# Performance work log

Hardware: AMD Instinct MI355X
Metric: run time of the kernel (lower is better)

Reference implementation:

```python
import jax, jax.numpy as jnp
import numpy as np

N_ATOMS = 100_000
N_EDGES = 1_600_000
N_RADIAL = 16
N_ELEM = 119          # periodic table size used by per-element scale/shift
HIDDEN = 512
N_FEAT = N_RADIAL + N_RADIAL * N_RADIAL  # M0 + M1-contraction features = 272
R_CUT = 5.0
EPS = 1e-8


def setup_inputs() -> dict:
    key = jax.random.key(0)
    ks = jax.random.split(key, 10)
    R = jax.random.normal(ks[0], (N_ATOMS, 3), jnp.float32)
    Z = jax.random.randint(ks[1], (N_ATOMS,), 0, N_ELEM).astype(jnp.int32)
    idx = jax.random.randint(ks[2], (2, N_EDGES), 0, N_ATOMS)
    box = jnp.zeros((3, 3), jnp.float32)
    offsets = jnp.zeros((N_EDGES, 3), jnp.float32)
    # descriptor params: Gaussian radial basis centers / width
    centers = jnp.linspace(0.0, R_CUT, N_RADIAL, dtype=jnp.float32)
    width = jnp.asarray(0.5, jnp.float32)
    # readout MLP params
    W1 = jax.random.normal(ks[3], (N_FEAT, HIDDEN), jnp.float32) / np.sqrt(N_FEAT)
    b1 = jnp.zeros((HIDDEN,), jnp.float32)
    W2 = jax.random.normal(ks[4], (HIDDEN, HIDDEN), jnp.float32) / np.sqrt(HIDDEN)
    b2 = jnp.zeros((HIDDEN,), jnp.float32)
    W3 = jax.random.normal(ks[5], (HIDDEN, 1), jnp.float32) / np.sqrt(HIDDEN)
    b3 = jnp.zeros((1,), jnp.float32)
    # per-element scale/shift
    scale = jnp.ones((N_ELEM,), jnp.float32)
    shift = jax.random.normal(ks[6], (N_ELEM,), jnp.float32)
    return {"R": R, "Z": Z, "idx": idx, "box": box, "offsets": offsets,
            "centers": centers, "width": width,
            "W1": W1, "b1": b1, "W2": W2, "b2": b2, "W3": W3, "b3": b3,
            "scale": scale, "shift": shift}


def reference(R, Z, idx, box, offsets, centers, width,
              W1, b1, W2, b2, W3, b3, scale, shift):
    n = R.shape[0]
    idx_i, idx_j = idx[0], idx[1]
    # edge gather + free displacement (init_box == 0): dr = displacement(Rj, Ri) = Rj - Ri
    dr = R[idx_j] - R[idx_i]                      # (E, 3)
    r = jnp.linalg.norm(dr, axis=-1, keepdims=True)  # (E, 1)
    d = dr / (r + EPS)                            # unit directions (E, 3)
    # Gaussian radial basis (E, K)
    b = jnp.exp(-((r - centers[None, :]) ** 2) / (2.0 * width * width))
    # scatter-sum moments per atom
    M0 = jax.ops.segment_sum(b, idx_i, num_segments=n)                       # (N, K)
    M1 = jax.ops.segment_sum(b[:, :, None] * d[:, None, :], idx_i,
                             num_segments=n)                                 # (N, K, 3)
    # rotation-invariant gaussian-moment contraction
    G1 = jnp.einsum('nad,nbd->nab', M1, M1).reshape(n, -1)                   # (N, K*K)
    feat = jnp.concatenate([M0, G1], axis=-1)                                # (N, 272)
    # per-atom readout MLP (swish)
    h = jax.nn.silu(feat @ W1 + b1)
    h = jax.nn.silu(h @ W2 + b2)
    h = h @ W3 + b3                                                          # (N, 1)
    # per-element scale/shift, then total energy
    atomic_energies = scale[Z][:, None] * h + shift[Z][:, None]
    return jnp.sum(atomic_energies)
```

## Files before the change

kernel.cpp:

```cpp
#include <hip/hip_runtime.h>
#include <hip/hip_bf16.h>
#include <cstdint>

#define HID 512
#define K1P 288

typedef __attribute__((ext_vector_type(8))) short bf16x8;
typedef __attribute__((ext_vector_type(4))) float f32x4;

__device__ __forceinline__ short f2bf(float x) {
    __hip_bfloat16 h = __float2bfloat16(x);
    return *(short*)&h;
}
__device__ __forceinline__ float silu(float x) {
    return x * (1.0f / (1.0f + __expf(-x)));
}
__device__ __forceinline__ void gl_lds16(const void* src, void* dst) {
    __builtin_amdgcn_global_load_lds(
        (const __attribute__((address_space(1))) void*)src,
        (__attribute__((address_space(3))) void*)dst, 16, 0, 0);
}
__device__ __forceinline__ int xcd_swz(int bid, int nwg) {
    int q = nwg >> 3, r = nwg & 7;
    int xcd = bid & 7, i = bid >> 3;
    int base = (xcd < r) ? xcd * (q + 1) : r * (q + 1) + (xcd - r) * q;
    return base + i;
}

__global__ __launch_bounds__(256) void hist_kernel(
    const int* __restrict__ idx, int* __restrict__ counts, int nEdges)
{
    int e = blockIdx.x * 256 + threadIdx.x;
    if (e < nEdges) atomicAdd(&counts[idx[e]], 1);
}

__global__ __launch_bounds__(1024) void scan1_kernel(
    const int* __restrict__ counts, int* __restrict__ starts,
    int* __restrict__ blockSum, int n)
{
    __shared__ int wsum[16];
    int t = threadIdx.x, lane = t & 63, wid = t >> 6;
    int i = blockIdx.x * 1024 + t;
    int v = (i < n) ? counts[i] : 0;
    int incl = v;
    #pragma unroll
    for (int off = 1; off < 64; off <<= 1) {
        int u = __shfl_up(incl, off);
        if (lane >= off) incl += u;
    }
    if (lane == 63) wsum[wid] = incl;
    __syncthreads();
    if (t < 16) {
        int s = wsum[t];
        #pragma unroll
        for (int off = 1; off < 16; off <<= 1) {
            int u = __shfl_up(s, off);
            if (t >= off) s += u;
        }
        wsum[t] = s;
    }
    __syncthreads();
    int woff = (wid == 0) ? 0 : wsum[wid - 1];
    if (i < n) starts[i] = woff + incl - v;
    if (t == 0) blockSum[blockIdx.x] = wsum[15];
}

__global__ __launch_bounds__(1024) void scan2_kernel(
    const int* __restrict__ blockSum, int* __restrict__ blockOff,
    int* __restrict__ starts, int nb, int n)
{
    __shared__ int arr[1024];
    int t = threadIdx.x;
    int v = (t < nb) ? blockSum[t] : 0;
    arr[t] = v;
    __syncthreads();
    #pragma unroll
    for (int off = 1; off < 1024; off <<= 1) {
        int x = (t >= off) ? arr[t - off] : 0;
        __syncthreads();
        arr[t] += x;
        __syncthreads();
    }
    if (t < nb) blockOff[t] = arr[t] - v;
    if (t == 0) starts[n] = arr[nb - 1];
}

__global__ __launch_bounds__(1024) void scan3_kernel(
    int* __restrict__ starts, int* __restrict__ cursor,
    const int* __restrict__ blockOff, int n)
{
    int i = blockIdx.x * 1024 + threadIdx.x;
    if (i < n) {
        int s = starts[i] + blockOff[blockIdx.x];
        starts[i] = s;
        cursor[i] = s;
    }
}

__global__ __launch_bounds__(256) void scatter_kernel(
    const float* __restrict__ R, const int* __restrict__ idx,
    int* __restrict__ cursor, float4* __restrict__ sorted, int nEdges)
{
    int e = blockIdx.x * 256 + threadIdx.x;
    if (e >= nEdges) return;
    int i = idx[e];
    int j = idx[nEdges + e];
    float rix = R[3*(size_t)i], riy = R[3*(size_t)i+1], riz = R[3*(size_t)i+2];
    float rjx = R[3*(size_t)j], rjy = R[3*(size_t)j+1], rjz = R[3*(size_t)j+2];
    float dx = rjx - rix, dy = rjy - riy, dz = rjz - riz;
    float r = sqrtf(dx*dx + dy*dy + dz*dz);
    float inv = 1.0f / (r + 1e-8f);
    int pos = atomicAdd(&cursor[i], 1);
    sorted[pos] = make_float4(r, dx*inv, dy*inv, dz*inv);
}

__global__ __launch_bounds__(256) void accum_kernel(
    const float4* __restrict__ sorted, const int* __restrict__ starts,
    const float* __restrict__ centers, const float* __restrict__ width,
    float* __restrict__ M0M1, int nAtoms)
{
    int wv = threadIdx.x >> 6, lane = threadIdx.x & 63;
    int atom = blockIdx.x * 4 + wv;
    if (atom >= nAtoms) return;
    int s = starts[atom], e = starts[atom + 1];
    int k = lane >> 2, c = lane & 3;
    float ck = centers[k];
    float w = width[0];
    float inv2w2 = 1.0f / (2.0f * w * w);
    float acc = 0.0f;
    auto term = [&](float4 v) {
        float diff = v.x - ck;
        float b = __expf(-diff * diff * inv2w2);
        float comp = (c == 0) ? 1.0f : ((c == 1) ? v.y : ((c == 2) ? v.z : v.w));
        return b * comp;
    };
    int p = s;
    for (; p + 3 < e; p += 4) {
        float4 v0 = sorted[p];
        float4 v1 = sorted[p + 1];
        float4 v2 = sorted[p + 2];
        float4 v3 = sorted[p + 3];
        acc += term(v0); acc += term(v1); acc += term(v2); acc += term(v3);
    }
    for (; p < e; ++p) acc += term(sorted[p]);
    M0M1[(size_t)atom * 64 + lane] = acc;
}

__global__ __launch_bounds__(256) void convW_kernel(
    const float* __restrict__ W, short* __restrict__ Wt, int K, int Kpad, int N)
{
    int n = blockIdx.x * 256 + threadIdx.x;
    int k = blockIdx.y;
    if (n >= N) return;
    float v = (k < K) ? W[(size_t)k * N + n] : 0.0f;
    Wt[(size_t)n * Kpad + k] = f2bf(v);
}

__global__ __launch_bounds__(256, 2) void gemm1_mfma(
    const float* __restrict__ M0M1, const short* __restrict__ W1t,
    const float* __restrict__ bias, short* __restrict__ C, int M, int nwg)
{
    __shared__ float MsT[64][128];
    __shared__ short Asl[2][4096];
    __shared__ short Bsl[4][4096];
    int t = threadIdx.x;
    int w = t >> 6, lane = t & 63;
    int wr = w >> 1, wc = w & 1;
    int li = lane & 15, lg = lane >> 4;
    int lin = xcd_swz(blockIdx.x, nwg);
    int row0 = (lin >> 2) * 128;
    int col0 = (lin & 3) * 128;

    {
        int mrow = t >> 1, mo = (t & 1) * 32;
        int gm = row0 + mrow; if (gm > M - 1) gm = M - 1;
        const float4* src = (const float4*)(M0M1 + (size_t)gm * 64 + mo);
        #pragma unroll
        for (int q = 0; q < 8; ++q) {
            float4 v = src[q];
            int c0 = mo + q * 4;
            MsT[c0+0][mrow] = v.x; MsT[c0+1][mrow] = v.y;
            MsT[c0+2][mrow] = v.z; MsT[c0+3][mrow] = v.w;
        }
    }
    __syncthreads();

    auto stageA = [&](int kt, int buf) {
        #pragma unroll
        for (int p = 0; p < 2; ++p) {
            int cell = p * 256 + t;
            int k8 = cell >> 7, row = cell & 127;
            int kbase = kt * 32 + k8 * 8;
            bf16x8 v;
            if (kbase < 16) {
                #pragma unroll
                for (int j = 0; j < 8; ++j) v[j] = f2bf(MsT[4*(kbase+j)][row]);
            } else if (kbase < 272) {
                int g = kbase - 16, a = g >> 4, b0 = g & 15;
                float ax = MsT[4*a+1][row], ay = MsT[4*a+2][row], az = MsT[4*a+3][row];
                #pragma unroll
                for (int j = 0; j < 8; ++j) {
                    int b = b0 + j;
                    v[j] = f2bf(ax*MsT[4*b+1][row] + ay*MsT[4*b+2][row] + az*MsT[4*b+3][row]);
                }
            } else {
                #pragma unroll
                for (int j = 0; j < 8; ++j) v[j] = 0;
            }
            *(bf16x8*)&Asl[buf][cell * 8] = v;
        }
    };
    auto stageB = [&](int kt, int buf) {
        #pragma unroll
        for (int p = 0; p < 2; ++p) {
            int cell = p * 256 + t;
            int k8 = cell >> 7, col = cell & 127;
            const short* src = W1t + (size_t)(col0 + col) * K1P + kt*32 + k8*8;
            gl_lds16(src, &Bsl[buf][(p * 256 + w * 64) * 8]);
        }
    };

    f32x4 acc[4][4] = {};
    const int NS = K1P / 32;
    stageA(0, 0);
    stageB(0, 0); stageB(1, 1); stageB(2, 2);

    #pragma unroll
    for (int s = 0; s < NS; ++s) {
        if (s <= NS - 3)      asm volatile("s_waitcnt vmcnt(4) lgkmcnt(0)\n\ts_barrier" ::: "memory");
        else if (s == NS - 2) asm volatile("s_waitcnt vmcnt(2) lgkmcnt(0)\n\ts_barrier" ::: "memory");
        else                  asm volatile("s_waitcnt vmcnt(0) lgkmcnt(0)\n\ts_barrier" ::: "memory");
        if (s + 3 < NS) stageB(s + 3, (s + 3) & 3);
        bf16x8 af[4], bfr[4];
        #pragma unroll
        for (int m = 0; m < 4; ++m)
            af[m] = *(const bf16x8*)&Asl[s & 1][(lg*128 + wr*64 + m*16 + li) * 8];
        #pragma unroll
        for (int n = 0; n < 4; ++n)
            bfr[n] = *(const bf16x8*)&Bsl[s & 3][(lg*128 + wc*64 + n*16 + li) * 8];
        if (s + 1 < NS) stageA(s + 1, (s + 1) & 1);
        __builtin_amdgcn_s_setprio(1);
        #pragma unroll
        for (int m = 0; m < 4; ++m)
            #pragma unroll
            for (int n = 0; n < 4; ++n)
                acc[m][n] = __builtin_amdgcn_mfma_f32_16x16x32_bf16(af[m], bfr[n], acc[m][n], 0, 0, 0);
        __builtin_amdgcn_s_setprio(0);
    }

    float bv[4];
    #pragma unroll
    for (int n = 0; n < 4; ++n) bv[n] = bias[col0 + wc*64 + n*16 + li];
    #pragma unroll
    for (int m = 0; m < 4; ++m)
        #pragma unroll
        for (int r = 0; r < 4; ++r) {
            int row = row0 + wr*64 + m*16 + lg*4 + r;
            if (row >= M) continue;
            size_t base = (size_t)row * HID + col0 + wc*64 + li;
            #pragma unroll
            for (int n = 0; n < 4; ++n) {
                float cx = acc[m][n][r] + bv[n];
                C[base + n*16] = f2bf(silu(cx));
            }
        }
}

__global__ __launch_bounds__(256, 2) void gemm2_mfma(
    const short* __restrict__ A, const short* __restrict__ W2t,
    const float* __restrict__ bias, const float* __restrict__ W3,
    const float* __restrict__ b3, const float* __restrict__ scale,
    const float* __restrict__ shift, const int* __restrict__ Z,
    float* __restrict__ out, int M, int nwg)
{
    __shared__ short Asl[4][4096];
    __shared__ short Bsl[4][4096];
    __shared__ float rsum[2][128];
    __shared__ float red[4];
    int t = threadIdx.x;
    int w = t >> 6, lane = t & 63;
    int wr = w >> 1, wc = w & 1;
    int li = lane & 15, lg = lane >> 4;
    int lin = xcd_swz(blockIdx.x, nwg);
    int row0 = (lin >> 2) * 128;
    int col0 = (lin & 3) * 128;

    auto stage = [&](int kt, int buf) {
        #pragma unroll
        for (int p = 0; p < 2; ++p) {
            int cell = p * 256 + t;
            int k8 = cell >> 7, row = cell & 127;
            int gr = row0 + row; if (gr > M - 1) gr = M - 1;
            const short* src = A + (size_t)gr * HID + kt*32 + k8*8;
            gl_lds16(src, &Asl[buf][(p * 256 + w * 64) * 8]);
        }
        #pragma unroll
        for (int p = 0; p < 2; ++p) {
            int cell = p * 256 + t;
            int k8 = cell >> 7, col = cell & 127;
            const short* src = W2t + (size_t)(col0 + col) * HID + kt*32 + k8*8;
            gl_lds16(src, &Bsl[buf][(p * 256 + w * 64) * 8]);
        }
    };

    f32x4 acc[4][4] = {};
    const int NS = HID / 32;
    stage(0, 0); stage(1, 1); stage(2, 2);

    for (int s = 0; s < NS; ++s) {
        if (s <= NS - 3)      asm volatile("s_waitcnt vmcnt(8)\n\ts_barrier" ::: "memory");
        else if (s == NS - 2) asm volatile("s_waitcnt vmcnt(4)\n\ts_barrier" ::: "memory");
        else                  asm volatile("s_waitcnt vmcnt(0)\n\ts_barrier" ::: "memory");
        if (s + 3 < NS) stage(s + 3, (s + 3) & 3);
        bf16x8 af[4], bfr[4];
        #pragma unroll
        for (int m = 0; m < 4; ++m)
            af[m] = *(const bf16x8*)&Asl[s & 3][(lg*128 + wr*64 + m*16 + li) * 8];
        #pragma unroll
        for (int n = 0; n < 4; ++n)
            bfr[n] = *(const bf16x8*)&Bsl[s & 3][(lg*128 + wc*64 + n*16 + li) * 8];
        __builtin_amdgcn_s_setprio(1);
        #pragma unroll
        for (int m = 0; m < 4; ++m)
            #pragma unroll
            for (int n = 0; n < 4; ++n)
                acc[m][n] = __builtin_amdgcn_mfma_f32_16x16x32_bf16(af[m], bfr[n], acc[m][n], 0, 0, 0);
        __builtin_amdgcn_s_setprio(0);
    }

    float bv[4], w3v[4];
    #pragma unroll
    for (int n = 0; n < 4; ++n) {
        int col = col0 + wc*64 + n*16 + li;
        bv[n]  = bias[col];
        w3v[n] = W3[col];
    }
    #pragma unroll
    for (int m = 0; m < 4; ++m)
        #pragma unroll
        for (int r = 0; r < 4; ++r) {
            float s = 0.f;
            #pragma unroll
            for (int n = 0; n < 4; ++n) {
                float cx = acc[m][n][r] + bv[n];
                s += silu(cx) * w3v[n];
            }
            #pragma unroll
            for (int off = 1; off < 16; off <<= 1) s += __shfl_xor(s, off);
            if (li == 0) rsum[wc][wr*64 + m*16 + lg*4 + r] = s;
        }
    __syncthreads();
    float e = 0.f;
    if (t < 128) {
        int row = row0 + t;
        if (row < M) {
            float v = rsum[0][t] + rsum[1][t];
            int z = Z[row];
            e = scale[z] * v;
            if ((lin & 3) == 0) e += scale[z] * b3[0] + shift[z];
        }
    }
    #pragma unroll
    for (int off = 32; off > 0; off >>= 1) e += __shfl_down(e, off);
    if (lane == 0) red[w] = e;
    __syncthreads();
    if (t == 0) atomicAdd(out, red[0] + red[1] + red[2] + red[3]);
}

extern "C" void kernel_launch(void* const* d_in, const int* in_sizes, int n_in,
                              void* d_out, int out_size, void* d_ws, size_t ws_size,
                              hipStream_t stream)
{
    const float* R       = (const float*)d_in[0];
    const int*   Z       = (const int*)  d_in[1];
    const int*   idx     = (const int*)  d_in[2];
    const float* centers = (const float*)d_in[5];
    const float* width   = (const float*)d_in[6];
    const float* W1      = (const float*)d_in[7];
    const float* b1      = (const float*)d_in[8];
    const float* W2      = (const float*)d_in[9];
    const float* b2      = (const float*)d_in[10];
    const float* W3      = (const float*)d_in[11];
    const float* b3      = (const float*)d_in[12];
    const float* scale   = (const float*)d_in[13];
    const float* shift   = (const float*)d_in[14];

    int nAtoms = in_sizes[0] / 3;
    int nEdges = in_sizes[2] / 2;

    size_t m0m1_b = (size_t)nAtoms * 64 * sizeof(float);
    size_t h1_b   = (size_t)nAtoms * HID * 2;
    size_t w1t_b  = (size_t)HID * K1P * 2;
    size_t w2t_b  = (size_t)HID * HID * 2;
    if (ws_size < m0m1_b + h1_b + w1t_b + w2t_b) return;

    char* ws = (char*)d_ws;
    float* M0M1 = (float*)ws;
    char*  regB = ws + m0m1_b;
    short* h1   = (short*)regB;
    short* W1t  = (short*)(ws + m0m1_b + h1_b);
    short* W2t  = W1t + (size_t)HID * K1P;

    int nb = (nAtoms + 1023) / 1024;
    size_t sorted_b = (size_t)nEdges * sizeof(float4);
    float4* sorted = (float4*)regB;
    int* counts   = (int*)(regB + sorted_b);
    int* starts   = counts + nAtoms;
    int* cursor   = starts + nAtoms + 1;
    int* blockSum = cursor + nAtoms;
    int* blockOff = blockSum + nb;
    if (sorted_b + (size_t)(3 * nAtoms + 1 + 2 * nb) * sizeof(int) > h1_b) return;

    float* out = (float*)d_out;

    hipMemsetAsync(counts, 0, (size_t)nAtoms * sizeof(int), stream);
    hipMemsetAsync(out, 0, sizeof(float), stream);

    convW_kernel<<<dim3(2, K1P), 256, 0, stream>>>(W1, W1t, 272, K1P, HID);
    convW_kernel<<<dim3(2, HID), 256, 0, stream>>>(W2, W2t, HID, HID, HID);

    int eb = (nEdges + 255) / 256;
    hist_kernel <<<eb, 256, 0, stream>>>(idx, counts, nEdges);
    scan1_kernel<<<nb, 1024, 0, stream>>>(counts, starts, blockSum, nAtoms);
    scan2_kernel<<<1, 1024, 0, stream>>>(blockSum, blockOff, starts, nb, nAtoms);
    scan3_kernel<<<nb, 1024, 0, stream>>>(starts, cursor, blockOff, nAtoms);
    scatter_kernel<<<eb, 256, 0, stream>>>(R, idx, cursor, sorted, nEdges);
    accum_kernel<<<(nAtoms + 3) / 4, 256, 0, stream>>>(sorted, starts, centers, width, M0M1, nAtoms);

    int gb = (nAtoms + 127) / 128;
    int nwg = gb * 4;
    gemm1_mfma<<<nwg, 256, 0, stream>>>(M0M1, W1t, b1, h1, nAtoms, nwg);
    gemm2_mfma<<<nwg, 256, 0, stream>>>(h1, W2t, b2, W3, b3, scale, shift, Z, out, nAtoms, nwg);
}
```

Baseline: 476.0 us.

## Make gemm2 persistent with LDS-resident W2 slice and register-streamed A rows

Replaces the tiled, multi-buffered gemm2 with a persistent kernel of 256 blocks of 512 threads. Each block loads its full 128-column slice of W2 (128 KB) into LDS once and then loops over row tiles. Each wave streams its own 16 A rows directly from global memory into registers, prefetching the next tile's first K chunks. This removes the per-tile LDS staging of both operands and the block barriers. Per-row energies are accumulated in registers and committed with one atomic per wave. The cost is a large LDS footprint (one block per CU) and uncoalesced per-lane A loads that bypass LDS.

```diff
diff --git a/kernel.cpp b/kernel.cpp
--- a/kernel.cpp
+++ b/kernel.cpp
@@ -266,105 +266,101 @@
         }
 }
 
-__global__ __launch_bounds__(256, 2) void gemm2_mfma(
+__global__ __launch_bounds__(512, 1) void gemm2_bres(
     const short* __restrict__ A, const short* __restrict__ W2t,
     const float* __restrict__ bias, const float* __restrict__ W3,
     const float* __restrict__ b3, const float* __restrict__ scale,
     const float* __restrict__ shift, const int* __restrict__ Z,
-    float* __restrict__ out, int M, int nwg)
-{
-    __shared__ short Asl[4][4096];
-    __shared__ short Bsl[4][4096];
-    __shared__ float rsum[2][128];
-    __shared__ float red[4];
+    float* __restrict__ out, int M, int T)
+{
+    __shared__ short Bp[8192 * 8];
     int t = threadIdx.x;
     int w = t >> 6, lane = t & 63;
-    int wr = w >> 1, wc = w & 1;
     int li = lane & 15, lg = lane >> 4;
-    int lin = xcd_swz(blockIdx.x, nwg);
-    int row0 = (lin >> 2) * 128;
+    int lin = xcd_swz(blockIdx.x, 256);
     int col0 = (lin & 3) * 128;
-
-    auto stage = [&](int kt, int buf) {
-        #pragma unroll
-        for (int p = 0; p < 2; ++p) {
-            int cell = p * 256 + t;
-            int k8 = cell >> 7, row = cell & 127;
-            int gr = row0 + row; if (gr > M - 1) gr = M - 1;
-            const short* src = A + (size_t)gr * HID + kt*32 + k8*8;
-            gl_lds16(src, &Asl[buf][(p * 256 + w * 64) * 8]);
-        }
-        #pragma unroll
-        for (int p = 0; p < 2; ++p) {
-            int cell = p * 256 + t;
-            int k8 = cell >> 7, col = cell & 127;
-            const short* src = W2t + (size_t)(col0 + col) * HID + kt*32 + k8*8;
-            gl_lds16(src, &Bsl[buf][(p * 256 + w * 64) * 8]);
-        }
-    };
-
-    f32x4 acc[4][4] = {};
-    const int NS = HID / 32;
-    stage(0, 0); stage(1, 1); stage(2, 2);
-
-    for (int s = 0; s < NS; ++s) {
-        if (s <= NS - 3)      asm volatile("s_waitcnt vmcnt(8)\n\ts_barrier" ::: "memory");
-        else if (s == NS - 2) asm volatile("s_waitcnt vmcnt(4)\n\ts_barrier" ::: "memory");
-        else                  asm volatile("s_waitcnt vmcnt(0)\n\ts_barrier" ::: "memory");
-        if (s + 3 < NS) stage(s + 3, (s + 3) & 3);
-        bf16x8 af[4], bfr[4];
-        #pragma unroll
-        for (int m = 0; m < 4; ++m)
-            af[m] = *(const bf16x8*)&Asl[s & 3][(lg*128 + wr*64 + m*16 + li) * 8];
-        #pragma unroll
-        for (int n = 0; n < 4; ++n)
-            bfr[n] = *(const bf16x8*)&Bsl[s & 3][(lg*128 + wc*64 + n*16 + li) * 8];
-        __builtin_amdgcn_s_setprio(1);
-        #pragma unroll
-        for (int m = 0; m < 4; ++m)
-            #pragma unroll
-            for (int n = 0; n < 4; ++n)
-                acc[m][n] = __builtin_amdgcn_mfma_f32_16x16x32_bf16(af[m], bfr[n], acc[m][n], 0, 0, 0);
-        __builtin_amdgcn_s_setprio(0);
-    }
-
-    float bv[4], w3v[4];
-    #pragma unroll
-    for (int n = 0; n < 4; ++n) {
-        int col = col0 + wc*64 + n*16 + li;
+    int rg = lin >> 2;
+
+    #pragma unroll
+    for (int i = 0; i < 16; ++i) {
+        int cell = i * 512 + t;
+        int c = cell >> 9, k8 = (cell >> 7) & 3, col = cell & 127;
+        const short* src = W2t + (size_t)(col0 + col) * HID + c * 32 + k8 * 8;
+        gl_lds16(src, &Bp[(i * 512 + w * 64) * 8]);
+    }
+    asm volatile("s_waitcnt vmcnt(0)" ::: "memory");
+    __syncthreads();
+
+    float bv[8], w3v[8];
+    #pragma unroll
+    for (int n = 0; n < 8; ++n) {
+        int col = col0 + n * 16 + li;
         bv[n]  = bias[col];
         w3v[n] = W3[col];
     }
-    #pragma unroll
-    for (int m = 0; m < 4; ++m)
+    float b30 = b3[0];
+    float ew = 0.f;
+
+    const short* arowCur;
+    {
+        int gr = rg * 128 + w * 16 + li; if (gr > M - 1) gr = M - 1;
+        arowCur = A + (size_t)gr * HID + lg * 8;
+    }
+    bf16x8 aw0 = *(const bf16x8*)(arowCur +  0);
+    bf16x8 aw1 = *(const bf16x8*)(arowCur + 32);
+    bf16x8 aw2 = *(const bf16x8*)(arowCur + 64);
+    bf16x8 aw3 = *(const bf16x8*)(arowCur + 96);
+
+    for (int rt = rg; rt < T; rt += 64) {
+        int row0w = rt * 128 + w * 16;
+        const short* arowNext;
+        {
+            int rtn = (rt + 64 < T) ? rt + 64 : rt;
+            int gr = rtn * 128 + w * 16 + li; if (gr > M - 1) gr = M - 1;
+            arowNext = A + (size_t)gr * HID + lg * 8;
+        }
+        f32x4 acc[8] = {};
+        #pragma unroll
+        for (int kt = 0; kt < 16; ++kt) {
+            bf16x8 a = (kt & 3) == 0 ? aw0 : (kt & 3) == 1 ? aw1 : (kt & 3) == 2 ? aw2 : aw3;
+            bf16x8 bfr[8];
+            #pragma unroll
+            for (int n = 0; n < 8; ++n)
+                bfr[n] = *(const bf16x8*)&Bp[((kt*4 + lg)*128 + n*16 + li) * 8];
+            bf16x8 nxt;
+            if (kt < 12) nxt = *(const bf16x8*)(arowCur + (kt + 4) * 32);
+            else         nxt = *(const bf16x8*)(arowNext + (kt - 12) * 32);
+            #pragma unroll
+            for (int n = 0; n < 8; ++n)
+                acc[n] = __builtin_amdgcn_mfma_f32_16x16x32_bf16(a, bfr[n], acc[n], 0, 0, 0);
+            if ((kt & 3) == 0) aw0 = nxt; else if ((kt & 3) == 1) aw1 = nxt;
+            else if ((kt & 3) == 2) aw2 = nxt; else aw3 = nxt;
+        }
+        arowCur = arowNext;
         #pragma unroll
         for (int r = 0; r < 4; ++r) {
             float s = 0.f;
             #pragma unroll
-            for (int n = 0; n < 4; ++n) {
-                float cx = acc[m][n][r] + bv[n];
+            for (int n = 0; n < 8; ++n) {
+                float cx = acc[n][r] + bv[n];
                 s += silu(cx) * w3v[n];
             }
-            #pragma unroll
-            for (int off = 1; off < 16; off <<= 1) s += __shfl_xor(s, off);
-            if (li == 0) rsum[wc][wr*64 + m*16 + lg*4 + r] = s;
-        }
-    __syncthreads();
-    float e = 0.f;
-    if (t < 128) {
-        int row = row0 + t;
-        if (row < M) {
-            float v = rsum[0][t] + rsum[1][t];
-            int z = Z[row];
-            e = scale[z] * v;
-            if ((lin & 3) == 0) e += scale[z] * b3[0] + shift[z];
-        }
-    }
-    #pragma unroll
-    for (int off = 32; off > 0; off >>= 1) e += __shfl_down(e, off);
-    if (lane == 0) red[w] = e;
-    __syncthreads();
-    if (t == 0) atomicAdd(out, red[0] + red[1] + red[2] + red[3]);
+            s += __shfl_xor(s, 1);
+            s += __shfl_xor(s, 2);
+            s += __shfl_xor(s, 4);
+            s += __shfl_xor(s, 8);
+            int row = row0w + lg*4 + r;
+            if (li == 0 && row < M) {
+                int z = Z[row];
+                float e = scale[z] * s;
+                if (col0 == 0) e += scale[z] * b30 + shift[z];
+                ew += e;
+            }
+        }
+    }
+    #pragma unroll
+    for (int off = 32; off > 0; off >>= 1) ew += __shfl_down(ew, off);
+    if (lane == 0) atomicAdd(out, ew);
 }
 
 extern "C" void kernel_launch(void* const* d_in, const int* in_sizes, int n_in,
@@ -430,5 +426,6 @@
     int gb = (nAtoms + 127) / 128;
     int nwg = gb * 4;
     gemm1_mfma<<<nwg, 256, 0, stream>>>(M0M1, W1t, b1, h1, nAtoms, nwg);
-    gemm2_mfma<<<nwg, 256, 0, stream>>>(h1, W2t, b2, W3, b3, scale, shift, Z, out, nAtoms, nwg);
-}
+    int T = gb;
+    gemm2_bres<<<256, 512, 0, stream>>>(h1, W2t, b2, W3, b3, scale, shift, Z, out, nAtoms, T);
+}
```

Result: slower. 873.3 us (+83.5%).

## Double-buffer MFMA operand registers and deepen LDS prefetch in both GEMMs

Applied to the files above, without the earlier changes.

Both GEMM kernels now load the next k-step's A/B fragments from LDS into a second register buffer while the current step's MFMAs run. The aim is to hide LDS read latency behind matrix math. gemm1 gets a third A LDS buffer so A can be staged two steps ahead, and the vmcnt waits are tightened to match. This raises register and LDS use, which may lower occupancy, and the waits must cover the earlier reads.

```diff
diff --git a/kernel.cpp b/kernel.cpp
--- a/kernel.cpp
+++ b/kernel.cpp
@@ -161,7 +161,7 @@
     const float* __restrict__ bias, short* __restrict__ C, int M, int nwg)
 {
     __shared__ float MsT[64][128];
-    __shared__ short Asl[2][4096];
+    __shared__ short Asl[3][4096];
     __shared__ short Bsl[4][4096];
     int t = threadIdx.x;
     int w = t >> 6, lane = t & 63;
@@ -221,30 +221,38 @@
     };
 
     f32x4 acc[4][4] = {};
+    bf16x8 afs[2][4], bfs[2][4];
     const int NS = K1P / 32;
-    stageA(0, 0);
+    stageA(0, 0); stageA(1, 1);
     stageB(0, 0); stageB(1, 1); stageB(2, 2);
+    asm volatile("s_waitcnt vmcnt(4) lgkmcnt(0)\n\ts_barrier" ::: "memory");
+    #pragma unroll
+    for (int m = 0; m < 4; ++m)
+        afs[0][m] = *(const bf16x8*)&Asl[0][(lg*128 + wr*64 + m*16 + li) * 8];
+    #pragma unroll
+    for (int n = 0; n < 4; ++n)
+        bfs[0][n] = *(const bf16x8*)&Bsl[0][(lg*128 + wc*64 + n*16 + li) * 8];
 
     #pragma unroll
     for (int s = 0; s < NS; ++s) {
-        if (s <= NS - 3)      asm volatile("s_waitcnt vmcnt(4) lgkmcnt(0)\n\ts_barrier" ::: "memory");
-        else if (s == NS - 2) asm volatile("s_waitcnt vmcnt(2) lgkmcnt(0)\n\ts_barrier" ::: "memory");
-        else                  asm volatile("s_waitcnt vmcnt(0) lgkmcnt(0)\n\ts_barrier" ::: "memory");
+        if (s <= NS - 3) asm volatile("s_waitcnt vmcnt(2) lgkmcnt(0)\n\ts_barrier" ::: "memory");
+        else             asm volatile("s_waitcnt vmcnt(0) lgkmcnt(0)\n\ts_barrier" ::: "memory");
         if (s + 3 < NS) stageB(s + 3, (s + 3) & 3);
-        bf16x8 af[4], bfr[4];
+        if (s + 2 < NS) stageA(s + 2, (s + 2) % 3);
+        if (s + 1 < NS) {
+            #pragma unroll
+            for (int m = 0; m < 4; ++m)
+                afs[(s+1)&1][m] = *(const bf16x8*)&Asl[(s+1) % 3][(lg*128 + wr*64 + m*16 + li) * 8];
+            #pragma unroll
+            for (int n = 0; n < 4; ++n)
+                bfs[(s+1)&1][n] = *(const bf16x8*)&Bsl[(s+1) & 3][(lg*128 + wc*64 + n*16 + li) * 8];
+        }
+        __builtin_amdgcn_s_setprio(1);
         #pragma unroll
         for (int m = 0; m < 4; ++m)
-            af[m] = *(const bf16x8*)&Asl[s & 1][(lg*128 + wr*64 + m*16 + li) * 8];
-        #pragma unroll
-        for (int n = 0; n < 4; ++n)
-            bfr[n] = *(const bf16x8*)&Bsl[s & 3][(lg*128 + wc*64 + n*16 + li) * 8];
-        if (s + 1 < NS) stageA(s + 1, (s + 1) & 1);
-        __builtin_amdgcn_s_setprio(1);
-        #pragma unroll
-        for (int m = 0; m < 4; ++m)
             #pragma unroll
             for (int n = 0; n < 4; ++n)
-                acc[m][n] = __builtin_amdgcn_mfma_f32_16x16x32_bf16(af[m], bfr[n], acc[m][n], 0, 0, 0);
+                acc[m][n] = __builtin_amdgcn_mfma_f32_16x16x32_bf16(afs[s&1][m], bfs[s&1][n], acc[m][n], 0, 0, 0);
         __builtin_amdgcn_s_setprio(0);
     }
 
@@ -304,27 +312,36 @@
     };
 
     f32x4 acc[4][4] = {};
+    bf16x8 afs[2][4], bfs[2][4];
     const int NS = HID / 32;
     stage(0, 0); stage(1, 1); stage(2, 2);
-
+    asm volatile("s_waitcnt vmcnt(8)\n\ts_barrier" ::: "memory");
+    #pragma unroll
+    for (int m = 0; m < 4; ++m)
+        afs[0][m] = *(const bf16x8*)&Asl[0][(lg*128 + wr*64 + m*16 + li) * 8];
+    #pragma unroll
+    for (int n = 0; n < 4; ++n)
+        bfs[0][n] = *(const bf16x8*)&Bsl[0][(lg*128 + wc*64 + n*16 + li) * 8];
+
+    #pragma unroll
     for (int s = 0; s < NS; ++s) {
-        if (s <= NS - 3)      asm volatile("s_waitcnt vmcnt(8)\n\ts_barrier" ::: "memory");
-        else if (s == NS - 2) asm volatile("s_waitcnt vmcnt(4)\n\ts_barrier" ::: "memory");
-        else                  asm volatile("s_waitcnt vmcnt(0)\n\ts_barrier" ::: "memory");
+        if (s <= NS - 3) asm volatile("s_waitcnt vmcnt(4)\n\ts_barrier" ::: "memory");
+        else             asm volatile("s_waitcnt vmcnt(0)\n\ts_barrier" ::: "memory");
         if (s + 3 < NS) stage(s + 3, (s + 3) & 3);
-        bf16x8 af[4], bfr[4];
+        if (s + 1 < NS) {
+            #pragma unroll
+            for (int m = 0; m < 4; ++m)
+                afs[(s+1)&1][m] = *(const bf16x8*)&Asl[(s+1) & 3][(lg*128 + wr*64 + m*16 + li) * 8];
+            #pragma unroll
+            for (int n = 0; n < 4; ++n)
+                bfs[(s+1)&1][n] = *(const bf16x8*)&Bsl[(s+1) & 3][(lg*128 + wc*64 + n*16 + li) * 8];
+        }
+        __builtin_amdgcn_s_setprio(1);
         #pragma unroll
         for (int m = 0; m < 4; ++m)
-            af[m] = *(const bf16x8*)&Asl[s & 3][(lg*128 + wr*64 + m*16 + li) * 8];
-        #pragma unroll
-        for (int n = 0; n < 4; ++n)
-            bfr[n] = *(const bf16x8*)&Bsl[s & 3][(lg*128 + wc*64 + n*16 + li) * 8];
-        __builtin_amdgcn_s_setprio(1);
-        #pragma unroll
-        for (int m = 0; m < 4; ++m)
             #pragma unroll
             for (int n = 0; n < 4; ++n)
-                acc[m][n] = __builtin_amdgcn_mfma_f32_16x16x32_bf16(af[m], bfr[n], acc[m][n], 0, 0, 0);
+                acc[m][n] = __builtin_amdgcn_mfma_f32_16x16x32_bf16(afs[s&1][m], bfs[s&1][n], acc[m][n], 0, 0, 0);
         __builtin_amdgcn_s_setprio(0);
     }
 
```

Result: slower. 523.1 us (+9.9%).

## Fuse moment contraction into accum kernel and feed bf16 features to GEMM1

Applied to the files above, without the earlier changes.

The accum kernel now builds the full 288-wide bf16 feature row (M0 plus the M1·M1 contraction) per atom through shared memory and writes it to a new workspace buffer. A new gemm_feat kernel streams that buffer with a 4-stage global_load_lds pipeline, replacing gemm1's on-the-fly feature construction from fp32 M0M1. This removes the contraction work that was redundant across the four column tiles of GEMM1, at the cost of writing and reading an extra ~57MB of features. The path only runs if the workspace is large enough, otherwise it falls back to the old code.

```diff
diff --git a/kernel.cpp b/kernel.cpp
--- a/kernel.cpp
+++ b/kernel.cpp
@@ -117,8 +117,10 @@
 __global__ __launch_bounds__(256) void accum_kernel(
     const float4* __restrict__ sorted, const int* __restrict__ starts,
     const float* __restrict__ centers, const float* __restrict__ width,
-    float* __restrict__ M0M1, int nAtoms)
-{
+    float* __restrict__ M0M1, short* __restrict__ feat16,
+    int nAtoms, int useFeat)
+{
+    __shared__ float sm[4][64];
     int wv = threadIdx.x >> 6, lane = threadIdx.x & 63;
     int atom = blockIdx.x * 4 + wv;
     if (atom >= nAtoms) return;
@@ -143,7 +145,31 @@
         acc += term(v0); acc += term(v1); acc += term(v2); acc += term(v3);
     }
     for (; p < e; ++p) acc += term(sorted[p]);
-    M0M1[(size_t)atom * 64 + lane] = acc;
+
+    if (!useFeat) {
+        M0M1[(size_t)atom * 64 + lane] = acc;
+        return;
+    }
+    sm[wv][lane] = acc;
+    asm volatile("s_waitcnt lgkmcnt(0)" ::: "memory");
+    short* frow = feat16 + (size_t)atom * K1P;
+    #pragma unroll
+    for (int q = 0; q < 5; ++q) {
+        int idx5 = q * 64 + lane;
+        if (idx5 >= K1P) break;
+        float val;
+        if (idx5 < 16) {
+            val = sm[wv][4 * idx5];
+        } else if (idx5 < 272) {
+            int g = idx5 - 16, a = g >> 4, b = g & 15;
+            val = sm[wv][4*a+1] * sm[wv][4*b+1]
+                + sm[wv][4*a+2] * sm[wv][4*b+2]
+                + sm[wv][4*a+3] * sm[wv][4*b+3];
+        } else {
+            val = 0.0f;
+        }
+        frow[idx5] = f2bf(val);
+    }
 }
 
 __global__ __launch_bounds__(256) void convW_kernel(
@@ -266,6 +292,82 @@
         }
 }
 
+__global__ __launch_bounds__(256, 2) void gemm_feat(
+    const short* __restrict__ F, const short* __restrict__ W1t,
+    const float* __restrict__ bias, short* __restrict__ C, int M, int nwg)
+{
+    __shared__ short Asl[4][4096];
+    __shared__ short Bsl[4][4096];
+    int t = threadIdx.x;
+    int w = t >> 6, lane = t & 63;
+    int wr = w >> 1, wc = w & 1;
+    int li = lane & 15, lg = lane >> 4;
+    int lin = xcd_swz(blockIdx.x, nwg);
+    int row0 = (lin >> 2) * 128;
+    int col0 = (lin & 3) * 128;
+
+    auto stage = [&](int kt, int buf) {
+        #pragma unroll
+        for (int p = 0; p < 2; ++p) {
+            int cell = p * 256 + t;
+            int k8 = cell >> 7, row = cell & 127;
+            int gr = row0 + row; if (gr > M - 1) gr = M - 1;
+            const short* src = F + (size_t)gr * K1P + kt*32 + k8*8;
+            gl_lds16(src, &Asl[buf][(p * 256 + w * 64) * 8]);
+        }
+        #pragma unroll
+        for (int p = 0; p < 2; ++p) {
+            int cell = p * 256 + t;
+            int k8 = cell >> 7, col = cell & 127;
+            const short* src = W1t + (size_t)(col0 + col) * K1P + kt*32 + k8*8;
+            gl_lds16(src, &Bsl[buf][(p * 256 + w * 64) * 8]);
+        }
+    };
+
+    f32x4 acc[4][4] = {};
+    const int NS = K1P / 32;
+    stage(0, 0); stage(1, 1); stage(2, 2);
+
+    #pragma unroll
+    for (int s = 0; s < NS; ++s) {
+        if (s <= NS - 3)      asm volatile("s_waitcnt vmcnt(8)\n\ts_barrier" ::: "memory");
+        else if (s == NS - 2) asm volatile("s_waitcnt vmcnt(4)\n\ts_barrier" ::: "memory");
+        else                  asm volatile("s_waitcnt vmcnt(0)\n\ts_barrier" ::: "memory");
+        if (s + 3 < NS) stage(s + 3, (s + 3) & 3);
+        bf16x8 af[4], bfr[4];
+        #pragma unroll
+        for (int m = 0; m < 4; ++m)
+            af[m] = *(const bf16x8*)&Asl[s & 3][(lg*128 + wr*64 + m*16 + li) * 8];
+        #pragma unroll
+        for (int n = 0; n < 4; ++n)
+            bfr[n] = *(const bf16x8*)&Bsl[s & 3][(lg*128 + wc*64 + n*16 + li) * 8];
+        __builtin_amdgcn_s_setprio(1);
+        #pragma unroll
+        for (int m = 0; m < 4; ++m)
+            #pragma unroll
+            for (int n = 0; n < 4; ++n)
+                acc[m][n] = __builtin_amdgcn_mfma_f32_16x16x32_bf16(af[m], bfr[n], acc[m][n], 0, 0, 0);
+        __builtin_amdgcn_s_setprio(0);
+    }
+
+    float bv[4];
+    #pragma unroll
+    for (int n = 0; n < 4; ++n) bv[n] = bias[col0 + wc*64 + n*16 + li];
+    #pragma unroll
+    for (int m = 0; m < 4; ++m)
+        #pragma unroll
+        for (int r = 0; r < 4; ++r) {
+            int row = row0 + wr*64 + m*16 + lg*4 + r;
+            if (row >= M) continue;
+            size_t base = (size_t)row * HID + col0 + wc*64 + li;
+            #pragma unroll
+            for (int n = 0; n < 4; ++n) {
+                float cx = acc[m][n][r] + bv[n];
+                C[base + n*16] = f2bf(silu(cx));
+            }
+        }
+}
+
 __global__ __launch_bounds__(256, 2) void gemm2_mfma(
     const short* __restrict__ A, const short* __restrict__ W2t,
     const float* __restrict__ bias, const float* __restrict__ W3,
@@ -392,14 +494,17 @@
     size_t h1_b   = (size_t)nAtoms * HID * 2;
     size_t w1t_b  = (size_t)HID * K1P * 2;
     size_t w2t_b  = (size_t)HID * HID * 2;
+    size_t feat_b = (size_t)nAtoms * K1P * 2;
     if (ws_size < m0m1_b + h1_b + w1t_b + w2t_b) return;
+    int useFeat = (ws_size >= m0m1_b + h1_b + w1t_b + w2t_b + feat_b) ? 1 : 0;
 
     char* ws = (char*)d_ws;
-    float* M0M1 = (float*)ws;
-    char*  regB = ws + m0m1_b;
-    short* h1   = (short*)regB;
-    short* W1t  = (short*)(ws + m0m1_b + h1_b);
-    short* W2t  = W1t + (size_t)HID * K1P;
+    float* M0M1  = (float*)ws;
+    char*  regB  = ws + m0m1_b;
+    short* h1    = (short*)regB;
+    short* W1t   = (short*)(ws + m0m1_b + h1_b);
+    short* W2t   = W1t + (size_t)HID * K1P;
+    short* feat16 = (short*)(ws + m0m1_b + h1_b + w1t_b + w2t_b);
 
     int nb = (nAtoms + 1023) / 1024;
     size_t sorted_b = (size_t)nEdges * sizeof(float4);
@@ -425,10 +530,14 @@
     scan2_kernel<<<1, 1024, 0, stream>>>(blockSum, blockOff, starts, nb, nAtoms);
     scan3_kernel<<<nb, 1024, 0, stream>>>(starts, cursor, blockOff, nAtoms);
     scatter_kernel<<<eb, 256, 0, stream>>>(R, idx, cursor, sorted, nEdges);
-    accum_kernel<<<(nAtoms + 3) / 4, 256, 0, stream>>>(sorted, starts, centers, width, M0M1, nAtoms);
+    accum_kernel<<<(nAtoms + 3) / 4, 256, 0, stream>>>(sorted, starts, centers, width,
+                                                       M0M1, feat16, nAtoms, useFeat);
 
     int gb = (nAtoms + 127) / 128;
     int nwg = gb * 4;
-    gemm1_mfma<<<nwg, 256, 0, stream>>>(M0M1, W1t, b1, h1, nAtoms, nwg);
+    if (useFeat)
+        gemm_feat<<<nwg, 256, 0, stream>>>(feat16, W1t, b1, h1, nAtoms, nwg);
+    else
+        gemm1_mfma<<<nwg, 256, 0, stream>>>(M0M1, W1t, b1, h1, nAtoms, nwg);
     gemm2_mfma<<<nwg, 256, 0, stream>>>(h1, W2t, b2, W3, b3, scale, shift, Z, out, nAtoms, nwg);
 }
```

New measurement: 470.1 us. No clear change (-1.2%).
